# Kernel optimization log

Measured on AMD Instinct MI355X. Metric: run time of the kernel, lower is better.

The kernel has to match this reference:

```python
import jax, jax.numpy as jnp
import numpy as np

INPUTS = 512    # feature dim per timestep == seq len T == max_length (required by module math)
HIDDEN = 512
OUTPUTS = 512
MAXLEN = INPUTS
BATCH = 256


def setup_inputs() -> dict:
    key = jax.random.key(0)
    ks = jax.random.split(key, 7)
    def lin(k, out_f, in_f):
        bound = 1.0 / np.sqrt(in_f)
        return jax.random.uniform(k, (out_f, in_f), jnp.float32, -bound, bound)
    return {
        "x": jax.random.normal(ks[0], (BATCH, INPUTS * MAXLEN), jnp.float32),
        "W_attn": lin(ks[1], MAXLEN, HIDDEN + INPUTS),
        "b_attn": jnp.zeros((MAXLEN,), jnp.float32),
        "W_comb": lin(ks[2], HIDDEN, INPUTS + MAXLEN),
        "b_comb": jnp.zeros((HIDDEN,), jnp.float32),
        "W_ih": lin(ks[3], 3 * HIDDEN, HIDDEN),
        "W_hh": lin(ks[4], 3 * HIDDEN, HIDDEN),
        "b_ih": jnp.zeros((3 * HIDDEN,), jnp.float32),
        "b_hh": jnp.zeros((3 * HIDDEN,), jnp.float32),
        "W_out": lin(ks[5], OUTPUTS, HIDDEN),
        "b_out": jnp.zeros((OUTPUTS,), jnp.float32),
    }


def reference(x, W_attn, b_attn, W_comb, b_comb, W_ih, W_hh, b_ih, b_hh, W_out, b_out):
    B = x.shape[0]
    H = HIDDEN
    xv = x.reshape(B, INPUTS, MAXLEN)      # [B, inputs, T]
    xs = jnp.transpose(xv, (2, 0, 1))      # [T, B, inputs] for scan over time

    def step(h, x_t):
        # Bahdanau-style attention over the inputs axis (M == inputs)
        aw = jax.nn.softmax(jnp.concatenate([x_t, h], axis=1) @ W_attn.T + b_attn, axis=1)  # [B, M]
        ctx = jnp.einsum('bm,bmt->bt', aw, xv)                                              # [B, T]
        g = jax.nn.relu(jnp.concatenate([x_t, ctx], axis=1) @ W_comb.T + b_comb)            # [B, H]
        # PyTorch GRU cell, gate order (r, z, n)
        gi = g @ W_ih.T + b_ih
        gh = h @ W_hh.T + b_hh
        r = jax.nn.sigmoid(gi[:, :H] + gh[:, :H])
        z = jax.nn.sigmoid(gi[:, H:2 * H] + gh[:, H:2 * H])
        n = jnp.tanh(gi[:, 2 * H:] + r * gh[:, 2 * H:])
        h_new = (1.0 - z) * n + z * h
        return h_new, None

    h0 = jnp.zeros((B, H), x.dtype)
    hT, _ = jax.lax.scan(step, h0, xs)
    return hT @ W_out.T + b_out  # [B, outputs]
```

## Files before the change

kernel.cpp:

```cpp
#include <hip/hip_runtime.h>

#define NB 256
#define NT 512
#define NI 512
#define NH 512
#define NG 1536
#define NBLK 512

typedef __attribute__((ext_vector_type(8))) short bf16x8;
typedef __attribute__((ext_vector_type(4))) float f32x4;
typedef __attribute__((ext_vector_type(2))) float f32x2;

#define MFMA(a, b, c) __builtin_amdgcn_mfma_f32_16x16x32_bf16((a), (b), (c), 0, 0, 0)

#define BAR_LEAF(g)   ((g) * 64)
#define BAR_ROOT      1024
#define BAR_GEN       1088
#define FLG_LOGIT(rt) (1152 + (rt) * 64)
#define FLG_GH(rt)    (1664 + (rt) * 64)
#define FLG_XT        1920
#define FLG_G(rg)     (2176 + (rg) * 64)
#define FLG_GP(b)     (2688 + (b) * 64)
#define BAR_WORDS     20480

__device__ __forceinline__ unsigned short f2bf(float f) {
  unsigned int u = __float_as_uint(f);
  u = u + 0x7FFFu + ((u >> 16) & 1u);
  return (unsigned short)(u >> 16);
}
__device__ __forceinline__ float sigm(float x) { return 1.f / (1.f + __expf(-x)); }

__device__ __forceinline__ void stf(float* p, float v) {
  __hip_atomic_store(p, v, __ATOMIC_RELAXED, __HIP_MEMORY_SCOPE_AGENT);
}
__device__ __forceinline__ void stu32(void* p, unsigned v) {
  __hip_atomic_store((unsigned*)p, v, __ATOMIC_RELAXED, __HIP_MEMORY_SCOPE_AGENT);
}
__device__ __forceinline__ void stu64(void* p, unsigned long long v) {
  __hip_atomic_store((unsigned long long*)p, v, __ATOMIC_RELAXED, __HIP_MEMORY_SCOPE_AGENT);
}
__device__ __forceinline__ void ldg16(uint4& d, const void* p) {
  asm volatile("global_load_dwordx4 %0, %1, off sc1" : "=v"(d) : "v"(p));
}
__device__ __forceinline__ void ldg8(float2& d, const void* p) {
  asm volatile("global_load_dwordx2 %0, %1, off sc1" : "=v"(d) : "v"(p));
}
__device__ __forceinline__ void ldg4(float& d, const void* p) {
  asm volatile("global_load_dword %0, %1, off sc1" : "=v"(d) : "v"(p));
}
__device__ __forceinline__ void wait_vm0() {
  asm volatile("s_waitcnt vmcnt(0)" ::: "memory");
  __builtin_amdgcn_sched_barrier(0);
}
__device__ __forceinline__ bf16x8 as_frag(uint4 v) {
  union { uint4 u; bf16x8 f; } c; c.u = v; return c.f;
}

__device__ __forceinline__ void flag_add(unsigned* f) {
  __hip_atomic_fetch_add(f, 1u, __ATOMIC_RELAXED, __HIP_MEMORY_SCOPE_AGENT);
}
__device__ __forceinline__ void flag_wait(unsigned* f, unsigned target) {
  while (__hip_atomic_load(f, __ATOMIC_RELAXED, __HIP_MEMORY_SCOPE_AGENT) < target)
    __builtin_amdgcn_s_sleep(1);
}

#define FP8_FMA16(PX, A_, ACC) do {                                              \
    f32x2 d0 = __builtin_amdgcn_cvt_pk_f32_fp8((int)(PX).x, false);              \
    f32x2 d1 = __builtin_amdgcn_cvt_pk_f32_fp8((int)(PX).x, true);               \
    f32x2 d2 = __builtin_amdgcn_cvt_pk_f32_fp8((int)(PX).y, false);              \
    f32x2 d3 = __builtin_amdgcn_cvt_pk_f32_fp8((int)(PX).y, true);               \
    f32x2 d4 = __builtin_amdgcn_cvt_pk_f32_fp8((int)(PX).z, false);              \
    f32x2 d5 = __builtin_amdgcn_cvt_pk_f32_fp8((int)(PX).z, true);               \
    f32x2 d6 = __builtin_amdgcn_cvt_pk_f32_fp8((int)(PX).w, false);              \
    f32x2 d7 = __builtin_amdgcn_cvt_pk_f32_fp8((int)(PX).w, true);               \
    (ACC)[0]  = fmaf((A_), d0[0], (ACC)[0]);  (ACC)[1]  = fmaf((A_), d0[1], (ACC)[1]);  \
    (ACC)[2]  = fmaf((A_), d1[0], (ACC)[2]);  (ACC)[3]  = fmaf((A_), d1[1], (ACC)[3]);  \
    (ACC)[4]  = fmaf((A_), d2[0], (ACC)[4]);  (ACC)[5]  = fmaf((A_), d2[1], (ACC)[5]);  \
    (ACC)[6]  = fmaf((A_), d3[0], (ACC)[6]);  (ACC)[7]  = fmaf((A_), d3[1], (ACC)[7]);  \
    (ACC)[8]  = fmaf((A_), d4[0], (ACC)[8]);  (ACC)[9]  = fmaf((A_), d4[1], (ACC)[9]);  \
    (ACC)[10] = fmaf((A_), d5[0], (ACC)[10]); (ACC)[11] = fmaf((A_), d5[1], (ACC)[11]); \
    (ACC)[12] = fmaf((A_), d6[0], (ACC)[12]); (ACC)[13] = fmaf((A_), d6[1], (ACC)[13]); \
    (ACC)[14] = fmaf((A_), d7[0], (ACC)[14]); (ACC)[15] = fmaf((A_), d7[1], (ACC)[15]); \
  } while (0)

__global__ __launch_bounds__(256) void cast_f32_bf16(const float* __restrict__ s,
                                                     unsigned short* __restrict__ d, int n) {
  int i = blockIdx.x * 256 + threadIdx.x;
  int stride = gridDim.x * 256;
  for (; i < n; i += stride) d[i] = f2bf(s[i]);
}

__global__ __launch_bounds__(256) void zt_fp8(unsigned short* __restrict__ XZ,
                                              float* __restrict__ Zsc,
                                              const unsigned short* __restrict__ Wc) {
  __shared__ unsigned short As[32][552];
  __shared__ float Zf[32][512];
  const int tid = threadIdx.x;
  const int row0 = blockIdx.x * 32;
  const uint4* src = (const uint4*)(XZ + (size_t)row0 * 512);
#pragma unroll
  for (int it = 0; it < 8; ++it) {
    int e8 = tid + it * 256;
    uint4 v = src[e8];
    *(uint4*)&As[e8 >> 6][(e8 & 63) * 8] = v;
  }
  __syncthreads();
  const int lane = tid & 63, w = tid >> 6;
  const int al = lane & 15, kg = lane >> 4;
  const int rbase = (w & 1) * 16;
  const int cbase = (w >> 1) * 256;
  for (int cc = 0; cc < 16; ++cc) {
    int col0 = cbase + cc * 16;
    f32x4 acc = {0.f, 0.f, 0.f, 0.f};
    const unsigned short* Bp = Wc + (size_t)(col0 + al) * 1024 + 512;
    for (int k = 0; k < 512; k += 32) {
      bf16x8 av = *(const bf16x8*)&As[rbase + al][k + kg * 8];
      bf16x8 bv = *(const bf16x8*)(Bp + k + kg * 8);
      acc = MFMA(av, bv, acc);
    }
#pragma unroll
    for (int r = 0; r < 4; ++r)
      Zf[rbase + kg * 4 + r][col0 + al] = acc[r];
  }
  __syncthreads();
  unsigned char* Z8 = (unsigned char*)XZ + ((size_t)blockIdx.x << 15);
#pragma unroll 2
  for (int r8 = 0; r8 < 8; ++r8) {
    int row = w * 8 + r8;
    const float* vr = &Zf[row][lane * 8];
    float v0 = vr[0], v1 = vr[1], v2 = vr[2], v3 = vr[3];
    float v4 = vr[4], v5 = vr[5], v6 = vr[6], v7 = vr[7];
    float amax = fmaxf(fmaxf(fmaxf(fabsf(v0), fabsf(v1)), fmaxf(fabsf(v2), fabsf(v3))),
                       fmaxf(fmaxf(fabsf(v4), fabsf(v5)), fmaxf(fabsf(v6), fabsf(v7))));
#pragma unroll
    for (int off = 32; off >= 1; off >>= 1) amax = fmaxf(amax, __shfl_xor(amax, off));
    float inv = amax > 0.f ? 448.f / amax : 0.f;
    int w0 = __builtin_amdgcn_cvt_pk_fp8_f32(v0 * inv, v1 * inv, 0, false);
    w0 = __builtin_amdgcn_cvt_pk_fp8_f32(v2 * inv, v3 * inv, w0, true);
    int w1 = __builtin_amdgcn_cvt_pk_fp8_f32(v4 * inv, v5 * inv, 0, false);
    w1 = __builtin_amdgcn_cvt_pk_fp8_f32(v6 * inv, v7 * inv, w1, true);
    uint2 o; o.x = (unsigned)w0; o.y = (unsigned)w1;
    *(uint2*)(Z8 + ((size_t)row << 9) + lane * 8) = o;
    if (lane == 0) Zsc[row0 + row] = amax * (1.f / 448.f);
  }
}

__global__ __launch_bounds__(256) void init_kernel(const float* __restrict__ x,
                                                   unsigned short* __restrict__ Xt,
                                                   unsigned short* __restrict__ Hbf,
                                                   unsigned* __restrict__ bar) {
  int idx = blockIdx.x * 256 + threadIdx.x;
  if (idx < BAR_WORDS) bar[idx] = 0u;
  if (idx < NB * NI) {
    int b = idx >> 9, i = idx & 511;
    Xt[idx] = f2bf(x[((size_t)b * 512 + i) * 512]);
    Hbf[idx] = 0;
  }
}

__global__ __launch_bounds__(256) void lxgx0_kernel(const unsigned short* __restrict__ Xt0,
                                                    const unsigned short* __restrict__ Wa,
                                                    const unsigned short* __restrict__ Wc,
                                                    const float* __restrict__ b_comb,
                                                    float* __restrict__ Lx,
                                                    float* __restrict__ Gx) {
  const int tid = threadIdx.x, lane = tid & 63, w = tid >> 6;
  const int al = lane & 15, kg = lane >> 4;
  int T = blockIdx.x;
  int m = T >> 7, tt = T & 127;
  int rt = tt >> 4, ct = tt & 15;
  int row0 = rt * 32 + (w & 1) * 16, col0 = ct * 32 + (w >> 1) * 16;
  const unsigned short* A = Xt0 + (size_t)(row0 + al) * NI;
  const unsigned short* B = (m ? Wc : Wa) + (size_t)(col0 + al) * 1024;
  f32x4 acc = {0.f, 0.f, 0.f, 0.f};
  for (int k = 0; k < 512; k += 32)
    acc = MFMA(*(const bf16x8*)(A + k + kg * 8), *(const bf16x8*)(B + k + kg * 8), acc);
  float* dst = m ? Gx : Lx;
  float bias = m ? b_comb[col0 + al] : 0.f;
#pragma unroll
  for (int r = 0; r < 4; ++r) {
    int row = row0 + kg * 4 + r;
    dst[row * NI + col0 + al] = acc[r] + bias;
  }
}

struct KParams {
  const unsigned char* Z8;
  const float* Zsc;
  const unsigned short* Wa;
  const unsigned short* Whh;
  const unsigned short* Wc;
  const unsigned short* Wih;
  const unsigned short* Wout;
  unsigned short* Xt;
  unsigned short* Hbf;
  unsigned short* Gbf;
  float* logits;
  float* gh;
  float* Lx;
  float* Gx;
  float* Gp;
  const float* x;
  const float* b_attn;
  const float* b_hh;
  const float* b_ih;
  const float* b_comb;
  const float* b_out;
  float* out;
  unsigned* bar;
};

__device__ __forceinline__ void gbar(unsigned* bar, unsigned gen_expect) {
  asm volatile("s_waitcnt vmcnt(0)" ::: "memory");
  __syncthreads();
  if (threadIdx.x == 0) {
    unsigned old = __hip_atomic_fetch_add(&bar[BAR_LEAF(blockIdx.x >> 5)], 1u,
                                          __ATOMIC_RELAXED, __HIP_MEMORY_SCOPE_AGENT);
    if ((old & 31) == 31) {
      unsigned ro = __hip_atomic_fetch_add(&bar[BAR_ROOT], 1u,
                                           __ATOMIC_RELAXED, __HIP_MEMORY_SCOPE_AGENT);
      if ((ro & 15) == 15)
        __hip_atomic_fetch_add(&bar[BAR_GEN], 1u,
                               __ATOMIC_RELAXED, __HIP_MEMORY_SCOPE_AGENT);
    }
    while (__hip_atomic_load(&bar[BAR_GEN], __ATOMIC_RELAXED, __HIP_MEMORY_SCOPE_AGENT) < gen_expect)
      __builtin_amdgcn_s_sleep(2);
    asm volatile("" ::: "memory");
  }
  __syncthreads();
}

__global__ __launch_bounds__(256, 2) void persistent_kernel(KParams P) {
  __shared__ __align__(16) unsigned char Zlds[65536];
  __shared__ float aw[512];
  __shared__ float pS[4][32][16];
  __shared__ float red[8];
  const int bid = blockIdx.x, tid = threadIdx.x;
  const int lane = tid & 63, w = tid >> 6;
  const int al = lane & 15, kg = lane >> 4;

  f32x4 hreg = {0.f, 0.f, 0.f, 0.f};

  const int b2_ = bid >> 1, mh_ = bid & 1;
  {
    const unsigned char* src = P.Z8 + ((size_t)(b2_ * 16 + mh_ * 8 + w * 2) << 15)
                               + (size_t)lane * 16;
    unsigned char* dst = &Zlds[w * 16384 + lane * 16];
#pragma unroll
    for (int k = 0; k < 16; ++k) {
      uint4 v = *(const uint4*)(src + ((size_t)k << 10));
      *(uint4*)(dst + (k << 10)) = v;
    }
  }
  uint4 px[16];
  {
    const unsigned char* Zb1 = P.Z8 + ((size_t)(b2_ * 16 + mh_ * 8 + w * 2 + 1) << 15)
                              + (size_t)lane * 16;
#pragma unroll
    for (int k = 0; k < 16; ++k) px[k] = *(const uint4*)(Zb1 + ((size_t)k << 10));
  }

  for (int t = 0; t < NT; ++t) {
    const int p = t & 1, np = p ^ 1;
    if (bid < 128) {
      int rt = bid >> 4, ct = bid & 15;
      int row0 = rt * 32 + (w & 1) * 16, col0 = ct * 32 + (w >> 1) * 16;
      const unsigned short* Ah = P.Hbf + (size_t)(row0 + al) * NH;
      const unsigned short* B = P.Wa + (size_t)(col0 + al) * 1024 + 512;
      uint4 fh[16];
      float lx[4];
#pragma unroll
      for (int i = 0; i < 16; ++i) ldg16(fh[i], Ah + i * 32 + kg * 8);
      {
        const float* lxp = P.Lx + (size_t)p * (NB * NI) + (size_t)(row0 + kg * 4) * NI + col0 + al;
#pragma unroll
        for (int r = 0; r < 4; ++r) ldg4(lx[r], lxp + (size_t)r * NI);
      }
      wait_vm0();
      f32x4 a1 = {0.f, 0.f, 0.f, 0.f};
#pragma unroll
      for (int i = 0; i < 16; ++i)
        a1 = MFMA(as_frag(fh[i]), *(const bf16x8*)(B + i * 32 + kg * 8), a1);
#pragma unroll
      for (int r = 0; r < 4; ++r) {
        int row = row0 + kg * 4 + r;
        stf(&P.logits[row * NI + col0 + al], lx[r] + a1[r] + P.b_attn[col0 + al]);
      }
      __syncthreads();
      if (tid == 0) flag_add(&P.bar[FLG_LOGIT(rt)]);
    } else if (bid < 320) {
      int bb = bid - 128;
      int rt = bb / 48, ct = bb % 48;
      int row0 = rt * 64 + w * 16, col0 = ct * 32;
      const unsigned short* Ah = P.Hbf + (size_t)(row0 + al) * NH;
      const unsigned short* B0 = P.Whh + (size_t)(col0 + al) * 512;
      const unsigned short* B1 = P.Whh + (size_t)(col0 + 16 + al) * 512;
      uint4 fa[16];
#pragma unroll
      for (int i = 0; i < 16; ++i) ldg16(fa[i], Ah + i * 32 + kg * 8);
      wait_vm0();
      f32x4 a0 = {0.f, 0.f, 0.f, 0.f}, a1 = {0.f, 0.f, 0.f, 0.f};
#pragma unroll
      for (int i = 0; i < 16; ++i) {
        a0 = MFMA(as_frag(fa[i]), *(const bf16x8*)(B0 + i * 32 + kg * 8), a0);
        a1 = MFMA(as_frag(fa[i]), *(const bf16x8*)(B1 + i * 32 + kg * 8), a1);
      }
#pragma unroll
      for (int r = 0; r < 4; ++r) {
        int row = row0 + kg * 4 + r;
        stf(&P.gh[row * NG + col0 + al], a0[r] + P.b_hh[col0 + al]);
        stf(&P.gh[row * NG + col0 + 16 + al], a1[r] + P.b_hh[col0 + 16 + al]);
      }
      __syncthreads();
      if (tid == 0) flag_add(&P.bar[FLG_GH(rt)]);
    } else if (bid < 384) {
    } else {
      if (t < NT - 1) {
        for (int e2 = (bid - 384) * 256 + tid; e2 < NB * NI / 2; e2 += 128 * 256) {
          int b = e2 >> 8, i = (e2 & 255) * 2;
          const float* xp = P.x + ((size_t)b * 512 + i) * 512 + t + 1;
          unsigned lo = f2bf(xp[0]);
          unsigned hi = f2bf(xp[512]);
          stu32(&P.Xt[(size_t)np * (NB * NI) + b * 512 + i], lo | (hi << 16));
        }
        __syncthreads();
        if (tid == 0) flag_add(&P.bar[FLG_XT]);
      }
    }

    {
      const int b = b2_, mh = mh_;
      if (tid == 0) flag_wait(&P.bar[FLG_LOGIT(b >> 5)], 16u * (t + 1));
      __syncthreads();
      float2 lv;
      ldg8(lv, P.logits + (size_t)b * NI + 2 * tid);
      wait_vm0();
      float mx = fmaxf(lv.x, lv.y);
#pragma unroll
      for (int off = 32; off >= 1; off >>= 1) mx = fmaxf(mx, __shfl_xor(mx, off));
      if (lane == 0) red[w] = mx;
      __syncthreads();
      mx = fmaxf(fmaxf(red[0], red[1]), fmaxf(red[2], red[3]));
      float e0 = __expf(lv.x - mx), e1 = __expf(lv.y - mx);
      float sm = e0 + e1;
#pragma unroll
      for (int off = 32; off >= 1; off >>= 1) sm += __shfl_xor(sm, off);
      if (lane == 0) red[4 + w] = sm;
      __syncthreads();
      sm = (red[4] + red[5]) + (red[6] + red[7]);
      float inv = 1.f / sm;
      float2 scl = *(const float2*)(P.Zsc + (size_t)b * 512 + 2 * tid);
      aw[2 * tid] = e0 * inv * scl.x;
      aw[2 * tid + 1] = e1 * inv * scl.y;
      __syncthreads();

      const int half = lane >> 5, hl = lane & 31;
      const float* awp = aw + mh * 256 + w * 64;
      float acc[16];
#pragma unroll
      for (int i = 0; i < 16; ++i) acc[i] = 0.f;
      const unsigned char* Zl = &Zlds[w * 16384 + lane * 16];
#pragma unroll
      for (int k = 0; k < 16; ++k) {
        uint4 pl = *(const uint4*)(Zl + (k << 10));
        float a_ = awp[2 * k + half];
        FP8_FMA16(pl, a_, acc);
      }
#pragma unroll
      for (int k = 0; k < 16; ++k) {
        float a_ = awp[32 + 2 * k + half];
        FP8_FMA16(px[k], a_, acc);
      }
#pragma unroll
      for (int i = 0; i < 16; ++i) acc[i] += __shfl_xor(acc[i], 32);
      if (lane < 32) {
#pragma unroll
        for (int i = 0; i < 16; ++i) pS[w][hl][i] = acc[i];
      }
      __syncthreads();
      const int c0 = 2 * tid, c1 = 2 * tid + 1;
      float s0 = (pS[0][c0 >> 4][c0 & 15] + pS[1][c0 >> 4][c0 & 15])
               + (pS[2][c0 >> 4][c0 & 15] + pS[3][c0 >> 4][c0 & 15]);
      float s1 = (pS[0][c1 >> 4][c1 & 15] + pS[1][c1 >> 4][c1 & 15])
               + (pS[2][c1 >> 4][c1 & 15] + pS[3][c1 >> 4][c1 & 15]);
      if (mh == 0) {
        union { float f[2]; unsigned long long q; } q0;
        q0.f[0] = s0; q0.f[1] = s1;
        stu64(&P.Gp[(size_t)b * NH + c0], q0.q);
        __syncthreads();
        if (tid == 0) flag_add(&P.bar[FLG_GP(b)]);
      } else {
        __syncthreads();
        if (tid == 0) flag_wait(&P.bar[FLG_GP(b)], (unsigned)(t + 1));
        __syncthreads();
        float2 gp2, gx2;
        ldg8(gp2, &P.Gp[(size_t)b * NH + c0]);
        ldg8(gx2, P.Gx + (size_t)p * (NB * NH) + (size_t)b * NH + c0);
        wait_vm0();
        float v0 = fmaxf(gx2.x + gp2.x + s0, 0.f);
        float v1 = fmaxf(gx2.y + gp2.y + s1, 0.f);
        stu32(&P.Gbf[(size_t)b * NH + c0], (unsigned)f2bf(v0) | ((unsigned)f2bf(v1) << 16));
        __syncthreads();
        if (tid == 0) flag_add(&P.bar[FLG_G(b >> 5)]);
      }
    }

    if (bid >= 384) {
      int q = bid - 384;
      int rt = q >> 4, ct = q & 15;
      int row0 = rt * 32 + (w & 1) * 16;
      int j0 = ct * 32 + (w >> 1) * 16;
      if (tid == 0) {
        flag_wait(&P.bar[FLG_G(rt)], 32u * (t + 1));
        flag_wait(&P.bar[FLG_GH(rt >> 1)], 48u * (t + 1));
      }
      __syncthreads();
      const unsigned short* Ag = P.Gbf + (size_t)(row0 + al) * NH;
      const unsigned short* Br = P.Wih + (size_t)(j0 + al) * 512;
      const unsigned short* Bz = P.Wih + (size_t)(j0 + 512 + al) * 512;
      const unsigned short* Bn = P.Wih + (size_t)(j0 + 1024 + al) * 512;
      int j = j0 + al;
      uint4 fa[16];
      float ghv[4][3];
#pragma unroll
      for (int i = 0; i < 16; ++i) ldg16(fa[i], Ag + i * 32 + kg * 8);
#pragma unroll
      for (int r = 0; r < 4; ++r) {
        const float* ghrow = P.gh + (size_t)(row0 + kg * 4 + r) * NG + j;
        ldg4(ghv[r][0], ghrow);
        ldg4(ghv[r][1], ghrow + 512);
        ldg4(ghv[r][2], ghrow + 1024);
      }
      wait_vm0();
      f32x4 ar = {0.f, 0.f, 0.f, 0.f}, az = {0.f, 0.f, 0.f, 0.f}, an = {0.f, 0.f, 0.f, 0.f};
#pragma unroll
      for (int i = 0; i < 16; ++i) {
        ar = MFMA(as_frag(fa[i]), *(const bf16x8*)(Br + i * 32 + kg * 8), ar);
        az = MFMA(as_frag(fa[i]), *(const bf16x8*)(Bz + i * 32 + kg * 8), az);
        an = MFMA(as_frag(fa[i]), *(const bf16x8*)(Bn + i * 32 + kg * 8), an);
      }
      float bir = P.b_ih[j], biz = P.b_ih[j + 512], bin_ = P.b_ih[j + 1024];
#pragma unroll
      for (int r = 0; r < 4; ++r) {
        int row = row0 + kg * 4 + r;
        float rg = sigm(ar[r] + bir + ghv[r][0]);
        float zg = sigm(az[r] + biz + ghv[r][1]);
        float ng = tanhf(an[r] + bin_ + rg * ghv[r][2]);
        float hn = (1.f - zg) * ng + zg * hreg[r];
        hreg[r] = hn;
        unsigned hv = f2bf(hn);
        unsigned ov = __shfl_xor((int)hv, 1);
        if ((al & 1) == 0)
          stu32(&P.Hbf[(size_t)row * NH + (j & ~1)], hv | (ov << 16));
      }
    } else if (bid >= 320) {
      if (t < NT - 1) {
        if (tid == 0) flag_wait(&P.bar[FLG_XT], 128u * (t + 1));
        __syncthreads();
        int q = bid - 320;
        for (int jj = 0; jj < 4; ++jj) {
          int T = q + 64 * jj;
          int m = T >> 7, tt = T & 127;
          int rt = tt >> 4, ct = tt & 15;
          int row0 = rt * 32 + (w & 1) * 16, col0 = ct * 32 + (w >> 1) * 16;
          const unsigned short* A = P.Xt + (size_t)np * (NB * NI) + (size_t)(row0 + al) * NI;
          const unsigned short* B = (m ? P.Wc : P.Wa) + (size_t)(col0 + al) * 1024;
          uint4 fa[16];
#pragma unroll
          for (int i = 0; i < 16; ++i) ldg16(fa[i], A + i * 32 + kg * 8);
          wait_vm0();
          f32x4 acc = {0.f, 0.f, 0.f, 0.f};
#pragma unroll
          for (int i = 0; i < 16; ++i)
            acc = MFMA(as_frag(fa[i]), *(const bf16x8*)(B + i * 32 + kg * 8), acc);
          float* dst = (m ? P.Gx : P.Lx) + (size_t)np * (NB * NI);
          float bias = m ? P.b_comb[col0 + al] : 0.f;
#pragma unroll
          for (int r = 0; r < 4; ++r) {
            int row = row0 + kg * 4 + r;
            stf(&dst[row * NI + col0 + al], acc[r] + bias);
          }
        }
      }
    }
    gbar(P.bar, (unsigned)(t + 1));
  }

  if (bid < 128) {
    int rt = bid >> 4, ct = bid & 15;
    int row0 = rt * 32 + (w & 1) * 16;
    int col0 = ct * 32 + (w >> 1) * 16;
    const unsigned short* Ah = P.Hbf + (size_t)(row0 + al) * NH;
    const unsigned short* B0 = P.Wout + (size_t)(col0 + al) * 512;
    uint4 fa[16];
#pragma unroll
    for (int i = 0; i < 16; ++i) ldg16(fa[i], Ah + i * 32 + kg * 8);
    wait_vm0();
    f32x4 acc = {0.f, 0.f, 0.f, 0.f};
#pragma unroll
    for (int i = 0; i < 16; ++i) acc = MFMA(as_frag(fa[i]), *(const bf16x8*)(B0 + i * 32 + kg * 8), acc);
#pragma unroll
    for (int r = 0; r < 4; ++r) {
      int row = row0 + kg * 4 + r;
      P.out[row * 512 + col0 + al] = acc[r] + P.b_out[col0 + al];
    }
  }
}

extern "C" void kernel_launch(void* const* d_in, const int* in_sizes, int n_in,
                              void* d_out, int out_size, void* d_ws, size_t ws_size,
                              hipStream_t stream) {
  const float* x      = (const float*)d_in[0];
  const float* W_attn = (const float*)d_in[1];
  const float* b_attn = (const float*)d_in[2];
  const float* W_comb = (const float*)d_in[3];
  const float* b_comb = (const float*)d_in[4];
  const float* W_ih   = (const float*)d_in[5];
  const float* W_hh   = (const float*)d_in[6];
  const float* b_ih   = (const float*)d_in[7];
  const float* b_hh   = (const float*)d_in[8];
  const float* W_out  = (const float*)d_in[9];
  const float* b_out  = (const float*)d_in[10];

  char* wp = (char*)d_ws;
  size_t off = 0;
  unsigned short* XZ   = (unsigned short*)(wp + off); off += (size_t)NB * NI * NH * 2;
  unsigned short* Wa   = (unsigned short*)(wp + off); off += (size_t)NI * 1024 * 2;
  unsigned short* Whh  = (unsigned short*)(wp + off); off += (size_t)NG * 512 * 2;
  unsigned short* Wc   = (unsigned short*)(wp + off); off += (size_t)NH * 1024 * 2;
  unsigned short* Wih  = (unsigned short*)(wp + off); off += (size_t)NG * 512 * 2;
  unsigned short* Wout = (unsigned short*)(wp + off); off += (size_t)512 * 512 * 2;
  unsigned short* Xt   = (unsigned short*)(wp + off); off += (size_t)2 * NB * NI * 2;
  unsigned short* Hbf  = (unsigned short*)(wp + off); off += (size_t)NB * NH * 2;
  unsigned short* Gbf  = (unsigned short*)(wp + off); off += (size_t)NB * NH * 2;
  float* logits        = (float*)(wp + off); off += (size_t)NB * NI * 4;
  float* gh            = (float*)(wp + off); off += (size_t)NB * NG * 4;
  float* Lx            = (float*)(wp + off); off += (size_t)2 * NB * NI * 4;
  float* Gx            = (float*)(wp + off); off += (size_t)2 * NB * NI * 4;
  float* Gp            = (float*)(wp + off); off += (size_t)NB * NH * 4;
  float* Zsc           = (float*)(wp + off); off += (size_t)NB * NI * 4;
  unsigned* bar        = (unsigned*)(wp + off); off += (size_t)BAR_WORDS * 4 + 4096;

  cast_f32_bf16<<<8192, 256, 0, stream>>>(x, XZ, NB * NI * NT);
  cast_f32_bf16<<<512, 256, 0, stream>>>(W_attn, Wa, NI * 1024);
  cast_f32_bf16<<<512, 256, 0, stream>>>(W_hh, Whh, NG * 512);
  cast_f32_bf16<<<512, 256, 0, stream>>>(W_comb, Wc, NH * 1024);
  cast_f32_bf16<<<512, 256, 0, stream>>>(W_ih, Wih, NG * 512);
  cast_f32_bf16<<<512, 256, 0, stream>>>(W_out, Wout, 512 * 512);
  zt_fp8<<<4096, 256, 0, stream>>>(XZ, Zsc, Wc);
  init_kernel<<<512, 256, 0, stream>>>(x, Xt, Hbf, bar);
  lxgx0_kernel<<<256, 256, 0, stream>>>(Xt, Wa, Wc, b_comb, Lx, Gx);

  KParams prm;
  prm.Z8 = (const unsigned char*)XZ; prm.Zsc = Zsc;
  prm.Wa = Wa; prm.Whh = Whh; prm.Wc = Wc; prm.Wih = Wih; prm.Wout = Wout;
  prm.Xt = Xt; prm.Hbf = Hbf; prm.Gbf = Gbf;
  prm.logits = logits; prm.gh = gh; prm.Lx = Lx; prm.Gx = Gx; prm.Gp = Gp;
  prm.x = x; prm.b_attn = b_attn; prm.b_hh = b_hh; prm.b_ih = b_ih; prm.b_out = b_out;
  prm.b_comb = b_comb;
  prm.out = (float*)d_out;
  prm.bar = bar;

  void* kargs[] = { &prm };
  hipError_t e = hipLaunchCooperativeKernel((const void*)persistent_kernel,
                                            dim3(NBLK), dim3(256), kargs, 0, stream);
  if (e != hipSuccess) {
    persistent_kernel<<<dim3(NBLK), dim3(256), 0, stream>>>(prm);
  }
}
```

Measured before the change: 26.94 ms.

## Pre-transpose all timesteps of x and drop per-step Xt gather and flag

Adds a tiled transpose kernel that converts x to bf16 laid out as [T][B*I] once before the recurrence, and moves the fp8 Z tensor into its own buffer so the bf16 copy survives. Inside the persistent kernel, the strided per-step gather of x by blocks 384+ and its FLG_XT flag are removed. Blocks 320+ now compute the next step's Lx/Gx projections earlier in the step, reading the pre-transposed slice with plain cached loads and no flag wait. The cost is an extra full-size transpose pass over x before the loop and more workspace memory.

```diff
diff --git a/kernel.cpp b/kernel.cpp
--- a/kernel.cpp
+++ b/kernel.cpp
@@ -18,7 +18,6 @@
 #define BAR_GEN       1088
 #define FLG_LOGIT(rt) (1152 + (rt) * 64)
 #define FLG_GH(rt)    (1664 + (rt) * 64)
-#define FLG_XT        1920
 #define FLG_G(rg)     (2176 + (rg) * 64)
 #define FLG_GP(b)     (2688 + (b) * 64)
 #define BAR_WORDS     20480
@@ -41,6 +40,9 @@
 }
 __device__ __forceinline__ void ldg16(uint4& d, const void* p) {
   asm volatile("global_load_dwordx4 %0, %1, off sc1" : "=v"(d) : "v"(p));
+}
+__device__ __forceinline__ void ldg16p(uint4& d, const void* p) {
+  asm volatile("global_load_dwordx4 %0, %1, off" : "=v"(d) : "v"(p));
 }
 __device__ __forceinline__ void ldg8(float2& d, const void* p) {
   asm volatile("global_load_dwordx2 %0, %1, off sc1" : "=v"(d) : "v"(p));
@@ -90,14 +92,15 @@
   for (; i < n; i += stride) d[i] = f2bf(s[i]);
 }
 
-__global__ __launch_bounds__(256) void zt_fp8(unsigned short* __restrict__ XZ,
+__global__ __launch_bounds__(256) void zt_fp8(const unsigned short* __restrict__ XZbf,
+                                              unsigned char* __restrict__ Z8c,
                                               float* __restrict__ Zsc,
                                               const unsigned short* __restrict__ Wc) {
   __shared__ unsigned short As[32][552];
   __shared__ float Zf[32][512];
   const int tid = threadIdx.x;
   const int row0 = blockIdx.x * 32;
-  const uint4* src = (const uint4*)(XZ + (size_t)row0 * 512);
+  const uint4* src = (const uint4*)(XZbf + (size_t)row0 * 512);
 #pragma unroll
   for (int it = 0; it < 8; ++it) {
     int e8 = tid + it * 256;
@@ -123,7 +126,7 @@
       Zf[rbase + kg * 4 + r][col0 + al] = acc[r];
   }
   __syncthreads();
-  unsigned char* Z8 = (unsigned char*)XZ + ((size_t)blockIdx.x << 15);
+  unsigned char* Z8 = Z8c + ((size_t)blockIdx.x << 14);
 #pragma unroll 2
   for (int r8 = 0; r8 < 8; ++r8) {
     int row = w * 8 + r8;
@@ -145,17 +148,28 @@
   }
 }
 
-__global__ __launch_bounds__(256) void init_kernel(const float* __restrict__ x,
-                                                   unsigned short* __restrict__ Xt,
-                                                   unsigned short* __restrict__ Hbf,
+__global__ __launch_bounds__(256) void xpose_kernel(const float* __restrict__ x,
+                                                    unsigned short* __restrict__ XtAll) {
+  __shared__ unsigned short T[64][66];
+  const int tid = threadIdx.x;
+  const int ri = blockIdx.x & 2047, ti = blockIdx.x >> 11;
+  const int R0 = ri * 64, T0 = ti * 64;
+  for (int e = tid; e < 4096; e += 256) {
+    int r = e >> 6, tt = e & 63;
+    T[r][tt] = f2bf(x[(size_t)(R0 + r) * 512 + T0 + tt]);
+  }
+  __syncthreads();
+  for (int e = tid; e < 4096; e += 256) {
+    int tt = e >> 6, r = e & 63;
+    XtAll[(size_t)(T0 + tt) * (NB * NI) + R0 + r] = T[r][tt];
+  }
+}
+
+__global__ __launch_bounds__(256) void init_kernel(unsigned short* __restrict__ Hbf,
                                                    unsigned* __restrict__ bar) {
   int idx = blockIdx.x * 256 + threadIdx.x;
   if (idx < BAR_WORDS) bar[idx] = 0u;
-  if (idx < NB * NI) {
-    int b = idx >> 9, i = idx & 511;
-    Xt[idx] = f2bf(x[((size_t)b * 512 + i) * 512]);
-    Hbf[idx] = 0;
-  }
+  if (idx < NB * NI) Hbf[idx] = 0;
 }
 
 __global__ __launch_bounds__(256) void lxgx0_kernel(const unsigned short* __restrict__ Xt0,
@@ -187,12 +201,12 @@
 struct KParams {
   const unsigned char* Z8;
   const float* Zsc;
+  const unsigned short* XtAll;
   const unsigned short* Wa;
   const unsigned short* Whh;
   const unsigned short* Wc;
   const unsigned short* Wih;
   const unsigned short* Wout;
-  unsigned short* Xt;
   unsigned short* Hbf;
   unsigned short* Gbf;
   float* logits;
@@ -200,7 +214,6 @@
   float* Lx;
   float* Gx;
   float* Gp;
-  const float* x;
   const float* b_attn;
   const float* b_hh;
   const float* b_ih;
@@ -243,7 +256,7 @@
 
   const int b2_ = bid >> 1, mh_ = bid & 1;
   {
-    const unsigned char* src = P.Z8 + ((size_t)(b2_ * 16 + mh_ * 8 + w * 2) << 15)
+    const unsigned char* src = P.Z8 + ((size_t)(b2_ * 16 + mh_ * 8 + w * 2) << 14)
                                + (size_t)lane * 16;
     unsigned char* dst = &Zlds[w * 16384 + lane * 16];
 #pragma unroll
@@ -254,7 +267,7 @@
   }
   uint4 px[16];
   {
-    const unsigned char* Zb1 = P.Z8 + ((size_t)(b2_ * 16 + mh_ * 8 + w * 2 + 1) << 15)
+    const unsigned char* Zb1 = P.Z8 + ((size_t)(b2_ * 16 + mh_ * 8 + w * 2 + 1) << 14)
                               + (size_t)lane * 16;
 #pragma unroll
     for (int k = 0; k < 16; ++k) px[k] = *(const uint4*)(Zb1 + ((size_t)k << 10));
@@ -314,17 +327,32 @@
       __syncthreads();
       if (tid == 0) flag_add(&P.bar[FLG_GH(rt)]);
     } else if (bid < 384) {
-    } else {
       if (t < NT - 1) {
-        for (int e2 = (bid - 384) * 256 + tid; e2 < NB * NI / 2; e2 += 128 * 256) {
-          int b = e2 >> 8, i = (e2 & 255) * 2;
-          const float* xp = P.x + ((size_t)b * 512 + i) * 512 + t + 1;
-          unsigned lo = f2bf(xp[0]);
-          unsigned hi = f2bf(xp[512]);
-          stu32(&P.Xt[(size_t)np * (NB * NI) + b * 512 + i], lo | (hi << 16));
+        int q = bid - 320;
+        const unsigned short* Xnp = P.XtAll + (size_t)(t + 1) * (NB * NI);
+        for (int jj = 0; jj < 4; ++jj) {
+          int T = q + 64 * jj;
+          int m = T >> 7, tt = T & 127;
+          int rt = tt >> 4, ct = tt & 15;
+          int row0 = rt * 32 + (w & 1) * 16, col0 = ct * 32 + (w >> 1) * 16;
+          const unsigned short* A = Xnp + (size_t)(row0 + al) * NI;
+          const unsigned short* B = (m ? P.Wc : P.Wa) + (size_t)(col0 + al) * 1024;
+          uint4 fa[16];
+#pragma unroll
+          for (int i = 0; i < 16; ++i) ldg16p(fa[i], A + i * 32 + kg * 8);
+          wait_vm0();
+          f32x4 acc = {0.f, 0.f, 0.f, 0.f};
+#pragma unroll
+          for (int i = 0; i < 16; ++i)
+            acc = MFMA(as_frag(fa[i]), *(const bf16x8*)(B + i * 32 + kg * 8), acc);
+          float* dst = (m ? P.Gx : P.Lx) + (size_t)np * (NB * NI);
+          float bias = m ? P.b_comb[col0 + al] : 0.f;
+#pragma unroll
+          for (int r = 0; r < 4; ++r) {
+            int row = row0 + kg * 4 + r;
+            stf(&dst[row * NI + col0 + al], acc[r] + bias);
+          }
         }
-        __syncthreads();
-        if (tid == 0) flag_add(&P.bar[FLG_XT]);
       }
     }
 
@@ -453,35 +481,6 @@
         if ((al & 1) == 0)
           stu32(&P.Hbf[(size_t)row * NH + (j & ~1)], hv | (ov << 16));
       }
-    } else if (bid >= 320) {
-      if (t < NT - 1) {
-        if (tid == 0) flag_wait(&P.bar[FLG_XT], 128u * (t + 1));
-        __syncthreads();
-        int q = bid - 320;
-        for (int jj = 0; jj < 4; ++jj) {
-          int T = q + 64 * jj;
-          int m = T >> 7, tt = T & 127;
-          int rt = tt >> 4, ct = tt & 15;
-          int row0 = rt * 32 + (w & 1) * 16, col0 = ct * 32 + (w >> 1) * 16;
-          const unsigned short* A = P.Xt + (size_t)np * (NB * NI) + (size_t)(row0 + al) * NI;
-          const unsigned short* B = (m ? P.Wc : P.Wa) + (size_t)(col0 + al) * 1024;
-          uint4 fa[16];
-#pragma unroll
-          for (int i = 0; i < 16; ++i) ldg16(fa[i], A + i * 32 + kg * 8);
-          wait_vm0();
-          f32x4 acc = {0.f, 0.f, 0.f, 0.f};
-#pragma unroll
-          for (int i = 0; i < 16; ++i)
-            acc = MFMA(as_frag(fa[i]), *(const bf16x8*)(B + i * 32 + kg * 8), acc);
-          float* dst = (m ? P.Gx : P.Lx) + (size_t)np * (NB * NI);
-          float bias = m ? P.b_comb[col0 + al] : 0.f;
-#pragma unroll
-          for (int r = 0; r < 4; ++r) {
-            int row = row0 + kg * 4 + r;
-            stf(&dst[row * NI + col0 + al], acc[r] + bias);
-          }
-        }
-      }
     }
     gbar(P.bar, (unsigned)(t + 1));
   }
@@ -524,13 +523,13 @@
 
   char* wp = (char*)d_ws;
   size_t off = 0;
-  unsigned short* XZ   = (unsigned short*)(wp + off); off += (size_t)NB * NI * NH * 2;
+  unsigned short* XZ   = (unsigned short*)(wp + off); off += (size_t)NB * NI * NT * 2;
+  unsigned char* Z8c   = (unsigned char*)(wp + off);  off += (size_t)NB * NI * 512;
   unsigned short* Wa   = (unsigned short*)(wp + off); off += (size_t)NI * 1024 * 2;
   unsigned short* Whh  = (unsigned short*)(wp + off); off += (size_t)NG * 512 * 2;
   unsigned short* Wc   = (unsigned short*)(wp + off); off += (size_t)NH * 1024 * 2;
   unsigned short* Wih  = (unsigned short*)(wp + off); off += (size_t)NG * 512 * 2;
   unsigned short* Wout = (unsigned short*)(wp + off); off += (size_t)512 * 512 * 2;
-  unsigned short* Xt   = (unsigned short*)(wp + off); off += (size_t)2 * NB * NI * 2;
   unsigned short* Hbf  = (unsigned short*)(wp + off); off += (size_t)NB * NH * 2;
   unsigned short* Gbf  = (unsigned short*)(wp + off); off += (size_t)NB * NH * 2;
   float* logits        = (float*)(wp + off); off += (size_t)NB * NI * 4;
@@ -541,22 +540,25 @@
   float* Zsc           = (float*)(wp + off); off += (size_t)NB * NI * 4;
   unsigned* bar        = (unsigned*)(wp + off); off += (size_t)BAR_WORDS * 4 + 4096;
 
+  unsigned short* XtAll = XZ;
+
   cast_f32_bf16<<<8192, 256, 0, stream>>>(x, XZ, NB * NI * NT);
   cast_f32_bf16<<<512, 256, 0, stream>>>(W_attn, Wa, NI * 1024);
   cast_f32_bf16<<<512, 256, 0, stream>>>(W_hh, Whh, NG * 512);
   cast_f32_bf16<<<512, 256, 0, stream>>>(W_comb, Wc, NH * 1024);
   cast_f32_bf16<<<512, 256, 0, stream>>>(W_ih, Wih, NG * 512);
   cast_f32_bf16<<<512, 256, 0, stream>>>(W_out, Wout, 512 * 512);
-  zt_fp8<<<4096, 256, 0, stream>>>(XZ, Zsc, Wc);
-  init_kernel<<<512, 256, 0, stream>>>(x, Xt, Hbf, bar);
-  lxgx0_kernel<<<256, 256, 0, stream>>>(Xt, Wa, Wc, b_comb, Lx, Gx);
+  zt_fp8<<<4096, 256, 0, stream>>>(XZ, Z8c, Zsc, Wc);
+  xpose_kernel<<<16384, 256, 0, stream>>>(x, XtAll);
+  init_kernel<<<512, 256, 0, stream>>>(Hbf, bar);
+  lxgx0_kernel<<<256, 256, 0, stream>>>(XtAll, Wa, Wc, b_comb, Lx, Gx);
 
   KParams prm;
-  prm.Z8 = (const unsigned char*)XZ; prm.Zsc = Zsc;
+  prm.Z8 = Z8c; prm.Zsc = Zsc; prm.XtAll = XtAll;
   prm.Wa = Wa; prm.Whh = Whh; prm.Wc = Wc; prm.Wih = Wih; prm.Wout = Wout;
-  prm.Xt = Xt; prm.Hbf = Hbf; prm.Gbf = Gbf;
+  prm.Hbf = Hbf; prm.Gbf = Gbf;
   prm.logits = logits; prm.gh = gh; prm.Lx = Lx; prm.Gx = Gx; prm.Gp = Gp;
-  prm.x = x; prm.b_attn = b_attn; prm.b_hh = b_hh; prm.b_ih = b_ih; prm.b_out = b_out;
+  prm.b_attn = b_attn; prm.b_hh = b_hh; prm.b_ih = b_ih; prm.b_out = b_out;
   prm.b_comb = b_comb;
   prm.out = (float*)d_out;
   prm.bar = bar;
```

Result: slower. 32.33 ms (+20.0%).

## Fuse attention-logit GEMV into per-row softmax blocks and widen W_hh tiles

Applied to the files above, without the earlier changes.

Each attention block now computes its own h·W_attn logits row with scalar bf16 FMAs from an LDS-staged hidden row. This removes the separate logit-producing block group, its global logits buffer and its flag wait. The W_hh gate GEMM is remapped onto 96 blocks with 64-column tiles (four MFMA accumulators each), and the flag count is adjusted to match. The cost is redundant scalar work: every one of the 512 blocks does a 512x512 GEMV per step, reading W_attn from global memory, which adds to the critical path in place of the MFMA-based version.

```diff
diff --git a/kernel.cpp b/kernel.cpp
--- a/kernel.cpp
+++ b/kernel.cpp
@@ -16,7 +16,6 @@
 #define BAR_LEAF(g)   ((g) * 64)
 #define BAR_ROOT      1024
 #define BAR_GEN       1088
-#define FLG_LOGIT(rt) (1152 + (rt) * 64)
 #define FLG_GH(rt)    (1664 + (rt) * 64)
 #define FLG_XT        1920
 #define FLG_G(rg)     (2176 + (rg) * 64)
@@ -28,6 +27,8 @@
   u = u + 0x7FFFu + ((u >> 16) & 1u);
   return (unsigned short)(u >> 16);
 }
+__device__ __forceinline__ float bflo(unsigned int p) { return __uint_as_float(p << 16); }
+__device__ __forceinline__ float bfhi(unsigned int p) { return __uint_as_float(p & 0xffff0000u); }
 __device__ __forceinline__ float sigm(float x) { return 1.f / (1.f + __expf(-x)); }
 
 __device__ __forceinline__ void stf(float* p, float v) {
@@ -195,7 +196,6 @@
   unsigned short* Xt;
   unsigned short* Hbf;
   unsigned short* Gbf;
-  float* logits;
   float* gh;
   float* Lx;
   float* Gx;
@@ -235,6 +235,7 @@
   __shared__ float aw[512];
   __shared__ float pS[4][32][16];
   __shared__ float red[8];
+  __shared__ __align__(16) unsigned short hrow[512];
   const int bid = blockIdx.x, tid = threadIdx.x;
   const int lane = tid & 63, w = tid >> 6;
   const int al = lane & 15, kg = lane >> 4;
@@ -262,59 +263,35 @@
 
   for (int t = 0; t < NT; ++t) {
     const int p = t & 1, np = p ^ 1;
-    if (bid < 128) {
-      int rt = bid >> 4, ct = bid & 15;
-      int row0 = rt * 32 + (w & 1) * 16, col0 = ct * 32 + (w >> 1) * 16;
+    if (bid >= 128 && bid < 224) {
+      int bb = bid - 128;
+      int rt = bb / 24, ct = bb % 24;
+      int row0 = rt * 64 + w * 16, col0 = ct * 64;
       const unsigned short* Ah = P.Hbf + (size_t)(row0 + al) * NH;
-      const unsigned short* B = P.Wa + (size_t)(col0 + al) * 1024 + 512;
-      uint4 fh[16];
-      float lx[4];
-#pragma unroll
-      for (int i = 0; i < 16; ++i) ldg16(fh[i], Ah + i * 32 + kg * 8);
-      {
-        const float* lxp = P.Lx + (size_t)p * (NB * NI) + (size_t)(row0 + kg * 4) * NI + col0 + al;
-#pragma unroll
-        for (int r = 0; r < 4; ++r) ldg4(lx[r], lxp + (size_t)r * NI);
-      }
-      wait_vm0();
-      f32x4 a1 = {0.f, 0.f, 0.f, 0.f};
-#pragma unroll
-      for (int i = 0; i < 16; ++i)
-        a1 = MFMA(as_frag(fh[i]), *(const bf16x8*)(B + i * 32 + kg * 8), a1);
-#pragma unroll
-      for (int r = 0; r < 4; ++r) {
-        int row = row0 + kg * 4 + r;
-        stf(&P.logits[row * NI + col0 + al], lx[r] + a1[r] + P.b_attn[col0 + al]);
-      }
-      __syncthreads();
-      if (tid == 0) flag_add(&P.bar[FLG_LOGIT(rt)]);
-    } else if (bid < 320) {
-      int bb = bid - 128;
-      int rt = bb / 48, ct = bb % 48;
-      int row0 = rt * 64 + w * 16, col0 = ct * 32;
-      const unsigned short* Ah = P.Hbf + (size_t)(row0 + al) * NH;
-      const unsigned short* B0 = P.Whh + (size_t)(col0 + al) * 512;
-      const unsigned short* B1 = P.Whh + (size_t)(col0 + 16 + al) * 512;
       uint4 fa[16];
 #pragma unroll
       for (int i = 0; i < 16; ++i) ldg16(fa[i], Ah + i * 32 + kg * 8);
       wait_vm0();
-      f32x4 a0 = {0.f, 0.f, 0.f, 0.f}, a1 = {0.f, 0.f, 0.f, 0.f};
+      f32x4 a[4] = {{0,0,0,0},{0,0,0,0},{0,0,0,0},{0,0,0,0}};
 #pragma unroll
       for (int i = 0; i < 16; ++i) {
-        a0 = MFMA(as_frag(fa[i]), *(const bf16x8*)(B0 + i * 32 + kg * 8), a0);
-        a1 = MFMA(as_frag(fa[i]), *(const bf16x8*)(B1 + i * 32 + kg * 8), a1);
-      }
-#pragma unroll
-      for (int r = 0; r < 4; ++r) {
-        int row = row0 + kg * 4 + r;
-        stf(&P.gh[row * NG + col0 + al], a0[r] + P.b_hh[col0 + al]);
-        stf(&P.gh[row * NG + col0 + 16 + al], a1[r] + P.b_hh[col0 + 16 + al]);
-      }
+        bf16x8 av = as_frag(fa[i]);
+#pragma unroll
+        for (int f = 0; f < 4; ++f) {
+          const unsigned short* B = P.Whh + (size_t)(col0 + f * 16 + al) * 512;
+          a[f] = MFMA(av, *(const bf16x8*)(B + i * 32 + kg * 8), a[f]);
+        }
+      }
+#pragma unroll
+      for (int f = 0; f < 4; ++f)
+#pragma unroll
+        for (int r = 0; r < 4; ++r) {
+          int row = row0 + kg * 4 + r;
+          stf(&P.gh[row * NG + col0 + f * 16 + al], a[f][r] + P.b_hh[col0 + f * 16 + al]);
+        }
       __syncthreads();
       if (tid == 0) flag_add(&P.bar[FLG_GH(rt)]);
-    } else if (bid < 384) {
-    } else {
+    } else if (bid >= 384) {
       if (t < NT - 1) {
         for (int e2 = (bid - 384) * 256 + tid; e2 < NB * NI / 2; e2 += 128 * 256) {
           int b = e2 >> 8, i = (e2 & 255) * 2;
@@ -330,11 +307,44 @@
 
     {
       const int b = b2_, mh = mh_;
-      if (tid == 0) flag_wait(&P.bar[FLG_LOGIT(b >> 5)], 16u * (t + 1));
-      __syncthreads();
+      {
+        float hv4;
+        ldg4(hv4, (const char*)(P.Hbf + (size_t)b * NH) + tid * 4);
+        wait_vm0();
+        ((float*)hrow)[tid] = hv4;
+      }
+      __syncthreads();
+      const int c0 = 2 * tid, c1 = c0 + 1;
+      float2 lxv;
+      ldg8(lxv, P.Lx + (size_t)p * (NB * NI) + (size_t)b * NI + c0);
+      float acc0 = 0.f, acc1 = 0.f;
+      {
+        const uint4* W0 = (const uint4*)(P.Wa + (size_t)c0 * 1024 + 512);
+        const uint4* W1 = (const uint4*)(P.Wa + (size_t)c1 * 1024 + 512);
+        const uint4* Hr = (const uint4*)hrow;
+#pragma unroll 8
+        for (int i = 0; i < 64; ++i) {
+          uint4 hu = Hr[i];
+          uint4 u0 = W0[i];
+          uint4 u1 = W1[i];
+          float h0 = bflo(hu.x), h1 = bfhi(hu.x), h2 = bflo(hu.y), h3 = bfhi(hu.y);
+          float h4 = bflo(hu.z), h5 = bfhi(hu.z), h6 = bflo(hu.w), h7 = bfhi(hu.w);
+          acc0 = fmaf(h0, bflo(u0.x), acc0); acc0 = fmaf(h1, bfhi(u0.x), acc0);
+          acc0 = fmaf(h2, bflo(u0.y), acc0); acc0 = fmaf(h3, bfhi(u0.y), acc0);
+          acc0 = fmaf(h4, bflo(u0.z), acc0); acc0 = fmaf(h5, bfhi(u0.z), acc0);
+          acc0 = fmaf(h6, bflo(u0.w), acc0); acc0 = fmaf(h7, bfhi(u0.w), acc0);
+          acc1 = fmaf(h0, bflo(u1.x), acc1); acc1 = fmaf(h1, bfhi(u1.x), acc1);
+          acc1 = fmaf(h2, bflo(u1.y), acc1); acc1 = fmaf(h3, bfhi(u1.y), acc1);
+          acc1 = fmaf(h4, bflo(u1.z), acc1); acc1 = fmaf(h5, bfhi(u1.z), acc1);
+          acc1 = fmaf(h6, bflo(u1.w), acc1); acc1 = fmaf(h7, bfhi(u1.w), acc1);
+        }
+      }
+      float ba0 = P.b_attn[c0], ba1 = P.b_attn[c1];
+      wait_vm0();
       float2 lv;
-      ldg8(lv, P.logits + (size_t)b * NI + 2 * tid);
-      wait_vm0();
+      lv.x = lxv.x + acc0 + ba0;
+      lv.y = lxv.y + acc1 + ba1;
+
       float mx = fmaxf(lv.x, lv.y);
 #pragma unroll
       for (int off = 32; off >= 1; off >>= 1) mx = fmaxf(mx, __shfl_xor(mx, off));
@@ -378,7 +388,6 @@
         for (int i = 0; i < 16; ++i) pS[w][hl][i] = acc[i];
       }
       __syncthreads();
-      const int c0 = 2 * tid, c1 = 2 * tid + 1;
       float s0 = (pS[0][c0 >> 4][c0 & 15] + pS[1][c0 >> 4][c0 & 15])
                + (pS[2][c0 >> 4][c0 & 15] + pS[3][c0 >> 4][c0 & 15]);
       float s1 = (pS[0][c1 >> 4][c1 & 15] + pS[1][c1 >> 4][c1 & 15])
@@ -412,7 +421,7 @@
       int j0 = ct * 32 + (w >> 1) * 16;
       if (tid == 0) {
         flag_wait(&P.bar[FLG_G(rt)], 32u * (t + 1));
-        flag_wait(&P.bar[FLG_GH(rt >> 1)], 48u * (t + 1));
+        flag_wait(&P.bar[FLG_GH(rt >> 1)], 24u * (t + 1));
       }
       __syncthreads();
       const unsigned short* Ag = P.Gbf + (size_t)(row0 + al) * NH;
@@ -533,7 +542,6 @@
   unsigned short* Xt   = (unsigned short*)(wp + off); off += (size_t)2 * NB * NI * 2;
   unsigned short* Hbf  = (unsigned short*)(wp + off); off += (size_t)NB * NH * 2;
   unsigned short* Gbf  = (unsigned short*)(wp + off); off += (size_t)NB * NH * 2;
-  float* logits        = (float*)(wp + off); off += (size_t)NB * NI * 4;
   float* gh            = (float*)(wp + off); off += (size_t)NB * NG * 4;
   float* Lx            = (float*)(wp + off); off += (size_t)2 * NB * NI * 4;
   float* Gx            = (float*)(wp + off); off += (size_t)2 * NB * NI * 4;
@@ -555,7 +563,7 @@
   prm.Z8 = (const unsigned char*)XZ; prm.Zsc = Zsc;
   prm.Wa = Wa; prm.Whh = Whh; prm.Wc = Wc; prm.Wih = Wih; prm.Wout = Wout;
   prm.Xt = Xt; prm.Hbf = Hbf; prm.Gbf = Gbf;
-  prm.logits = logits; prm.gh = gh; prm.Lx = Lx; prm.Gx = Gx; prm.Gp = Gp;
+  prm.gh = gh; prm.Lx = Lx; prm.Gx = Gx; prm.Gp = Gp;
   prm.x = x; prm.b_attn = b_attn; prm.b_hh = b_hh; prm.b_ih = b_ih; prm.b_out = b_out;
   prm.b_comb = b_comb;
   prm.out = (float*)d_out;
```

After: 48.88 ms. 81.4% more time.
